# Kernel tuning notes

Measured on AMD Instinct MI355X. Metric: run time of the kernel, lower is better.

The kernel has to match this reference:

```python
import jax, jax.numpy as jnp
import numpy as np

B, T, C, H = 128, 256, 384, 6
HS = C // H  # 64
EPS = 1e-5


def _ln(x, g, b):
    mu = jnp.mean(x, axis=-1, keepdims=True)
    var = jnp.mean(jnp.square(x - mu), axis=-1, keepdims=True)
    return (x - mu) * jax.lax.rsqrt(var + EPS) * g + b


def setup_inputs() -> dict:
    key = jax.random.key(0)
    ks = jax.random.split(key, 12)
    s = 0.02
    return {
        "x": jax.random.normal(ks[0], (B, T, C), jnp.float32),
        "wq": jax.random.normal(ks[1], (H, C, HS), jnp.float32) * s,
        "wk": jax.random.normal(ks[2], (H, C, HS), jnp.float32) * s,
        "wv": jax.random.normal(ks[3], (H, C, HS), jnp.float32) * s,
        "w_proj": jax.random.normal(ks[4], (C, C), jnp.float32) * s,
        "b_proj": jax.random.normal(ks[5], (C,), jnp.float32) * s,
        "w1": jax.random.normal(ks[6], (C, 4 * C), jnp.float32) * s,
        "b1": jax.random.normal(ks[7], (4 * C,), jnp.float32) * s,
        "w2": jax.random.normal(ks[8], (4 * C, C), jnp.float32) * s,
        "b2": jax.random.normal(ks[9], (C,), jnp.float32) * s,
        "ln1_g": 1.0 + jax.random.normal(ks[10], (C,), jnp.float32) * s,
        "ln1_b": jnp.zeros((C,), jnp.float32),
        "ln2_g": 1.0 + jax.random.normal(ks[11], (C,), jnp.float32) * s,
        "ln2_b": jnp.zeros((C,), jnp.float32),
    }


def reference(x, wq, wk, wv, w_proj, b_proj, w1, b1, w2, b2, ln1_g, ln1_b, ln2_g, ln2_b):
    # --- attention sublayer (dropout = identity, eval mode) ---
    h = _ln(x, ln1_g, ln1_b)                              # (B,T,C)
    q = jnp.einsum("btc,hcd->bhtd", h, wq)               # (B,H,T,HS)
    k = jnp.einsum("btc,hcd->bhtd", h, wk)
    v = jnp.einsum("btc,hcd->bhtd", h, wv)
    # NOTE: original scales by n_embed**-0.5 (C), not head_size**-0.5
    wei = jnp.einsum("bhtd,bhsd->bhts", q, k) * (C ** -0.5)  # (B,H,T,T)
    tril = jnp.tril(jnp.ones((T, T), bool))
    wei = jnp.where(tril, wei, -jnp.inf)
    # NOTE: original applies softmax over torch dim=1 of (B,T,T) = query axis
    wei = jax.nn.softmax(wei, axis=2)
    attn = jnp.einsum("bhts,bhsd->bhtd", wei, v)          # (B,H,T,HS)
    attn = attn.transpose(0, 2, 1, 3).reshape(B, T, C)    # head-concat order
    x = x + attn @ w_proj + b_proj
    # --- MLP sublayer ---
    h2 = _ln(x, ln2_g, ln2_b)
    x = x + jax.nn.relu(h2 @ w1 + b1) @ w2 + b2
    return x
```

## Files before the change

### kernel.cpp

```cpp
#include <hip/hip_runtime.h>

#define BB 128
#define TT 256
#define CCH 384
#define NHH 6
#define HSZ 64
#define BTT (BB*TT)
#define QKVLD 1152

typedef unsigned short u16;
typedef unsigned int   u32;
typedef __attribute__((ext_vector_type(8))) short  short8;
typedef __attribute__((ext_vector_type(4))) float  floatx4;

__device__ __forceinline__ u16 f2bf(float f) {
  union { float f; u32 i; } v; v.f = f; u32 x = v.i;
  return (u16)((x + 0x7fffu + ((x >> 16) & 1u)) >> 16);
}
__device__ __forceinline__ float bf2f(u16 w) {
  union { u32 i; float f; } v; v.i = ((u32)w) << 16; return v.f;
}

__device__ __forceinline__ void gll16(const u16* g, u16* l) {
  __builtin_amdgcn_global_load_lds((const __attribute__((address_space(1))) void*)g,
                                   (__attribute__((address_space(3))) void*)l, 16, 0, 0);
}

template <int INBF>
__global__ __launch_bounds__(256) void ln_kernel(const void* __restrict__ xv,
                                                 const float* __restrict__ g,
                                                 const float* __restrict__ b,
                                                 u16* __restrict__ out) {
  int row = blockIdx.x * 4 + (threadIdx.x >> 6);
  int lane = threadIdx.x & 63;
  float vals[6];
  float sum = 0.f;
  if (INBF) {
    const u16* xr = (const u16*)xv + (size_t)row * CCH;
#pragma unroll
    for (int i = 0; i < 6; ++i) { vals[i] = bf2f(xr[lane + (i << 6)]); sum += vals[i]; }
  } else {
    const float* xr = (const float*)xv + (size_t)row * CCH;
#pragma unroll
    for (int i = 0; i < 6; ++i) { vals[i] = xr[lane + (i << 6)]; sum += vals[i]; }
  }
#pragma unroll
  for (int off = 32; off; off >>= 1) sum += __shfl_xor(sum, off);
  float mean = sum * (1.f / 384.f);
  float vs = 0.f;
#pragma unroll
  for (int i = 0; i < 6; ++i) { float d = vals[i] - mean; vs += d * d; }
#pragma unroll
  for (int off = 32; off; off >>= 1) vs += __shfl_xor(vs, off);
  float rinv = rsqrtf(vs * (1.f / 384.f) + 1e-5f);
  u16* orow = out + (size_t)row * CCH;
#pragma unroll
  for (int i = 0; i < 6; ++i) {
    int c = lane + (i << 6);
    orow[c] = f2bf((vals[i] - mean) * rinv * g[c] + b[c]);
  }
}

__global__ __launch_bounds__(256) void prep_all(const float* __restrict__ wq,
                                                const float* __restrict__ wk,
                                                const float* __restrict__ wv,
                                                const float* __restrict__ wproj,
                                                const float* __restrict__ w1,
                                                const float* __restrict__ w2,
                                                u16* __restrict__ wqkv_t, u16* __restrict__ wp_t,
                                                u16* __restrict__ w1_t, u16* __restrict__ w2_t,
                                                const float* __restrict__ x,
                                                const float* __restrict__ ln1g,
                                                const float* __restrict__ ln1b,
                                                u16* __restrict__ h_out) {
  const int bidx = blockIdx.x;
  if (bidx < 6912) {
    int idx = bidx * 256 + threadIdx.x;
    const int S1 = 442368;
    const int S2 = S1 + 147456;
    const int S3 = S2 + 589824;
    const int S4 = S3 + 589824;
    if (idx < S1) {
      int i = idx, e = i & 7, l = (i >> 3) & 63, r = i >> 9;
      int kt = r % 12, nb = r / 12;
      int n = nb * 16 + (l & 15), k = kt * 32 + (l >> 4) * 8 + e;
      int sel = n / 384, nn = n % 384;
      size_t src = ((size_t)(nn >> 6) * 384 + k) * 64 + (nn & 63);
      float v = (sel == 0) ? wq[src] : (sel == 1) ? wk[src] : wv[src];
      wqkv_t[i] = f2bf(v);
    } else if (idx < S2) {
      int i = idx - S1, e = i & 7, l = (i >> 3) & 63, r = i >> 9;
      int kt = r % 12, nb = r / 12;
      int n = nb * 16 + (l & 15), k = kt * 32 + (l >> 4) * 8 + e;
      wp_t[i] = f2bf(wproj[(size_t)k * 384 + n]);
    } else if (idx < S3) {
      int i = idx - S2, e = i & 7, l = (i >> 3) & 63, r = i >> 9;
      int kt = r % 12, nb = r / 12;
      int n = nb * 16 + (l & 15), k = kt * 32 + (l >> 4) * 8 + e;
      w1_t[i] = f2bf(w1[(size_t)k * 1536 + n]);
    } else if (idx < S4) {
      int i = idx - S3, e = i & 7, l = (i >> 3) & 63, r = i >> 9;
      int kt = r % 48, nb = r / 48;
      int n = nb * 16 + (l & 15), k = kt * 32 + (l >> 4) * 8 + e;
      w2_t[i] = f2bf(w2[(size_t)k * 384 + n]);
    }
  } else {
    int row = (bidx - 6912) * 4 + (threadIdx.x >> 6);
    int lane = threadIdx.x & 63;
    const float* xr = x + (size_t)row * CCH;
    float vals[6];
    float sum = 0.f;
#pragma unroll
    for (int i = 0; i < 6; ++i) { vals[i] = xr[lane + (i << 6)]; sum += vals[i]; }
#pragma unroll
    for (int off = 32; off; off >>= 1) sum += __shfl_xor(sum, off);
    float mean = sum * (1.f / 384.f);
    float vs = 0.f;
#pragma unroll
    for (int i = 0; i < 6; ++i) { float d = vals[i] - mean; vs += d * d; }
#pragma unroll
    for (int off = 32; off; off >>= 1) vs += __shfl_xor(vs, off);
    float rinv = rsqrtf(vs * (1.f / 384.f) + 1e-5f);
    u16* orow = h_out + (size_t)row * CCH;
#pragma unroll
    for (int i = 0; i < 6; ++i) {
      int c = lane + (i << 6);
      orow[c] = f2bf((vals[i] - mean) * rinv * ln1g[c] + ln1b[c]);
    }
  }
}

template <int BIAS, int RES, int RELU, int OUTBF, int RESBF>
__global__ __launch_bounds__(192, 2) void gemm_kres3(const u16* __restrict__ A,
                                                     const u16* __restrict__ Bp,
                                                     const float* __restrict__ bias,
                                                     const void* __restrict__ resv,
                                                     void* __restrict__ outv,
                                                     int M, int N) {
  __shared__ __align__(16) u16 Ah[12 * 2048];
  const int tid = threadIdx.x;
  const int lane = tid & 63;
  const int w = tid >> 6;

  const int gx = gridDim.x;
  const int nwg = gx * gridDim.y;
  const int bid = blockIdx.y * gx + blockIdx.x;
  const int lin = (bid & 7) * (nwg >> 3) + (bid >> 3);
  const int m0 = (lin / gx) * 64, n0 = (lin % gx) * 192;

  const int lm = lane & 15, qd = lane >> 4;

#pragma unroll
  for (int g = 0; g < 16; ++g) {
    int call = w * 16 + g;
    int kt = call >> 2, c = call & 3;
    int row = 16 * c + (lane >> 2);
    int ch = (lane & 3) ^ ((row >> 1) & 3);
    const u16* src = A + (size_t)(m0 + row) * 384 + kt * 32 + ch * 8;
    gll16(src, &Ah[kt * 2048 + c * 512]);
  }

  const u16* bsrc[4];
#pragma unroll
  for (int j = 0; j < 4; ++j)
    bsrc[j] = Bp + ((size_t)((n0 >> 4) + 4 * w + j) * 12) * 512 + lane * 8;

  floatx4 acc[4][4];
  floatx4 zero4 = {0.f, 0.f, 0.f, 0.f};
#pragma unroll
  for (int i = 0; i < 4; ++i)
#pragma unroll
    for (int j = 0; j < 4; ++j) acc[i][j] = zero4;

  short8 bf[4][4];
#pragma unroll
  for (int j = 0; j < 4; ++j) bf[0][j] = *(const short8*)(bsrc[j]);
#pragma unroll
  for (int j = 0; j < 4; ++j) bf[1][j] = *(const short8*)(bsrc[j] + 512);
#pragma unroll
  for (int j = 0; j < 4; ++j) bf[2][j] = *(const short8*)(bsrc[j] + 1024);

  asm volatile("s_waitcnt vmcnt(0)" ::: "memory");
  __syncthreads();

#pragma unroll
  for (int kt = 0; kt < 12; ++kt) {
    if (kt + 3 < 12) {
      const int pb = (kt + 3) & 3;
#pragma unroll
      for (int j = 0; j < 4; ++j)
        bf[pb][j] = *(const short8*)(bsrc[j] + (kt + 3) * 512);
    }
    const int cb = kt & 3;
    short8 af[4];
#pragma unroll
    for (int i = 0; i < 4; ++i) {
      int rm = 16 * i + lm;
      af[i] = *(const short8*)&Ah[kt * 2048 + rm * 32 + (qd ^ ((rm >> 1) & 3)) * 8];
    }
#pragma unroll
    for (int i = 0; i < 4; ++i)
#pragma unroll
      for (int j = 0; j < 4; ++j)
        acc[i][j] = __builtin_amdgcn_mfma_f32_16x16x32_bf16(af[i], bf[cb][j], acc[i][j], 0, 0, 0);
  }

#pragma unroll
  for (int i = 0; i < 4; ++i) {
    int row0 = m0 + 16 * i + qd * 4;
#pragma unroll
    for (int j = 0; j < 4; ++j) {
      int col = n0 + 64 * w + 16 * j + lm;
      float bb = 0.f;
      if (BIAS) bb = bias[col];
#pragma unroll
      for (int r = 0; r < 4; ++r) {
        size_t idx = (size_t)(row0 + r) * N + col;
        float val = acc[i][j][r] + bb;
        if (RES) val += RESBF ? bf2f(((const u16*)resv)[idx]) : ((const float*)resv)[idx];
        if (RELU) val = fmaxf(val, 0.f);
        if (OUTBF) ((u16*)outv)[idx] = f2bf(val);
        else       ((float*)outv)[idx] = val;
      }
    }
  }
}

template <int BIAS, int RES, int RELU, int OUTBF, int RESBF>
__global__ __launch_bounds__(256, 3) void gemm_mfma(const u16* __restrict__ A,
                                                    const u16* __restrict__ Bp,
                                                    const float* __restrict__ bias,
                                                    const void* __restrict__ resv,
                                                    void* __restrict__ outv,
                                                    int M, int N, int K) {
  __shared__ __align__(16) u16 As[2][128 * 32];
  const int tid = threadIdx.x;
  const int lane = tid & 63;
  const int w = tid >> 6;
  const int wr = w >> 1, wc = w & 1;

  const int gx = gridDim.x;
  const int nwg = gx * gridDim.y;
  const int bid = blockIdx.y * gx + blockIdx.x;
  const int lin = (bid & 7) * (nwg >> 3) + (bid >> 3);
  const int m0 = (lin / gx) * 128, n0 = (lin % gx) * 128;

  const int lm = lane & 15, qd = lane >> 4;
  const int KT = K >> 5;

  floatx4 acc[4][4];
  floatx4 zero4 = {0.f, 0.f, 0.f, 0.f};
#pragma unroll
  for (int i = 0; i < 4; ++i)
#pragma unroll
    for (int j = 0; j < 4; ++j) acc[i][j] = zero4;

  const u16* srcA[2];
#pragma unroll
  for (int c = 0; c < 2; ++c) {
    int row = 32 * w + 16 * c + (lane >> 2);
    int ch = (lane & 3) ^ ((row >> 1) & 3);
    srcA[c] = A + (size_t)(m0 + row) * K + ch * 8;
  }
  const int dA = (32 * w) * 32;

  const u16* bsrc[4];
#pragma unroll
  for (int j = 0; j < 4; ++j)
    bsrc[j] = Bp + ((size_t)((n0 >> 4) + 4 * wc + j) * KT) * 512 + lane * 8;

#pragma unroll
  for (int c = 0; c < 2; ++c) gll16(srcA[c], &As[0][dA + 512 * c]);
  short8 bcur[4], bnxt[4];
#pragma unroll
  for (int j = 0; j < 4; ++j) bcur[j] = *(const short8*)(bsrc[j]);

  for (int k0 = 0; k0 < K; k0 += 64) {
    __syncthreads();
    {
      int kn = k0 + 32;
      int kto = (kn >> 5) << 9;
#pragma unroll
      for (int j = 0; j < 4; ++j) bnxt[j] = *(const short8*)(bsrc[j] + kto);
#pragma unroll
      for (int c = 0; c < 2; ++c) gll16(srcA[c] + kn, &As[1][dA + 512 * c]);
      short8 af[4];
#pragma unroll
      for (int i = 0; i < 4; ++i) {
        int rm = 64 * wr + 16 * i + lm;
        af[i] = *(const short8*)&As[0][rm * 32 + (qd ^ ((rm >> 1) & 3)) * 8];
      }
#pragma unroll
      for (int i = 0; i < 4; ++i)
#pragma unroll
        for (int j = 0; j < 4; ++j)
          acc[i][j] = __builtin_amdgcn_mfma_f32_16x16x32_bf16(af[i], bcur[j], acc[i][j], 0, 0, 0);
    }
    __syncthreads();
    {
      int kn = k0 + 64;
      if (kn < K) {
        int kto = (kn >> 5) << 9;
#pragma unroll
        for (int j = 0; j < 4; ++j) bcur[j] = *(const short8*)(bsrc[j] + kto);
#pragma unroll
        for (int c = 0; c < 2; ++c) gll16(srcA[c] + kn, &As[0][dA + 512 * c]);
      }
      short8 af[4];
#pragma unroll
      for (int i = 0; i < 4; ++i) {
        int rm = 64 * wr + 16 * i + lm;
        af[i] = *(const short8*)&As[1][rm * 32 + (qd ^ ((rm >> 1) & 3)) * 8];
      }
#pragma unroll
      for (int i = 0; i < 4; ++i)
#pragma unroll
        for (int j = 0; j < 4; ++j)
          acc[i][j] = __builtin_amdgcn_mfma_f32_16x16x32_bf16(af[i], bnxt[j], acc[i][j], 0, 0, 0);
    }
  }

#pragma unroll
  for (int i = 0; i < 4; ++i) {
    int row0 = m0 + 64 * wr + 16 * i + qd * 4;
#pragma unroll
    for (int j = 0; j < 4; ++j) {
      int col = n0 + 64 * wc + 16 * j + lm;
      float bb = 0.f;
      if (BIAS) bb = bias[col];
#pragma unroll
      for (int r = 0; r < 4; ++r) {
        size_t idx = (size_t)(row0 + r) * N + col;
        float val = acc[i][j][r] + bb;
        if (RES) val += RESBF ? bf2f(((const u16*)resv)[idx]) : ((const float*)resv)[idx];
        if (RELU) val = fmaxf(val, 0.f);
        if (OUTBF) ((u16*)outv)[idx] = f2bf(val);
        else       ((float*)outv)[idx] = val;
      }
    }
  }
}

#define ASCALE 0.051031036307982884f

__global__ __launch_bounds__(1024) void attn_mfma(const u16* __restrict__ qkv,
                                                  u16* __restrict__ out) {
  __shared__ __align__(16) char lds_raw[36864 + 20480 + 2048];
  u16*   Ks       = (u16*)lds_raw;
  u16*   VT       = (u16*)lds_raw;
  float* partials = (float*)(lds_raw + 36864);
  u16*   stage    = (u16*)(lds_raw + 36864);
  float* gmax     = (float*)(lds_raw + 57344);
  float* linv     = (float*)(lds_raw + 58368);

  const int tid = threadIdx.x;
  const int lane = tid & 63;
  const int w = tid >> 6;
  const int lm = lane & 15, qd = lane >> 4;
  const int b = blockIdx.x / NHH, h = blockIdx.x % NHH;
  const size_t rowbase = (size_t)b * TT;
  const u16* qp = qkv + rowbase * QKVLD + h * HSZ;
  const u16* kp = qp + 384;
  const u16* vp = qp + 768;

  {
    int s = tid >> 2, c4 = tid & 3;
    const u16* src = kp + (size_t)s * QKVLD;
    *(uint4*)&Ks[s * 72 + c4 * 8]       = *(const uint4*)(src + c4 * 8);
    *(uint4*)&Ks[s * 72 + (c4 + 4) * 8] = *(const uint4*)(src + (c4 + 4) * 8);
  }
  short8 qf0, qf1;
  {
    const u16* qrow = qp + (size_t)(16 * w + lm) * QKVLD + qd * 8;
    qf0 = *(const short8*)(qrow);
    qf1 = *(const short8*)(qrow + 32);
  }
  __syncthreads();

  floatx4 acc[16];
  floatx4 zero4 = {0.f, 0.f, 0.f, 0.f};
#pragma unroll
  for (int tc = 0; tc < 16; ++tc) acc[tc] = zero4;

#pragma unroll
  for (int tc = 0; tc < 16; ++tc) {
    if (tc <= w) {
      int sr = 16 * tc + lm;
      short8 kf0 = *(const short8*)&Ks[sr * 72 + qd * 8];
      short8 kf1 = *(const short8*)&Ks[sr * 72 + 32 + qd * 8];
      acc[tc] = __builtin_amdgcn_mfma_f32_16x16x32_bf16(qf0, kf0, acc[tc], 0, 0, 0);
      acc[tc] = __builtin_amdgcn_mfma_f32_16x16x32_bf16(qf1, kf1, acc[tc], 0, 0, 0);
    }
  }

  const int rb = 16 * w + qd * 4;
  float pmax[16];
#pragma unroll
  for (int tc = 0; tc < 16; ++tc) {
    float m = -1e30f;
    if (tc <= w) {
      int sc = 16 * tc + lm;
#pragma unroll
      for (int r = 0; r < 4; ++r) {
        float vv = acc[tc][r] * ASCALE;
        vv = (rb + r >= sc) ? vv : -1e30f;
        acc[tc][r] = vv;
        m = fmaxf(m, vv);
      }
    }
    m = fmaxf(m, __shfl_xor(m, 16));
    m = fmaxf(m, __shfl_xor(m, 32));
    pmax[tc] = m;
  }
  if (lane < 16) {
#pragma unroll
    for (int tc = 0; tc < 16; ++tc) partials[w * 256 + tc * 16 + lane] = pmax[tc];
  }
  __syncthreads();
  if (tid < 256) {
    float m = partials[tid];
#pragma unroll
    for (int i = 1; i < 16; ++i) m = fmaxf(m, partials[i * 256 + tid]);
    gmax[tid] = m;
  }
  __syncthreads();

  float psum[16];
#pragma unroll
  for (int tc = 0; tc < 16; ++tc) {
    float s = 0.f;
    if (tc <= w) {
      float gm = gmax[tc * 16 + lm];
#pragma unroll
      for (int r = 0; r < 4; ++r) {
        float e = (acc[tc][r] > -1e29f) ? __expf(acc[tc][r] - gm) : 0.f;
        acc[tc][r] = e;
        s += e;
      }
    }
    s += __shfl_xor(s, 16);
    s += __shfl_xor(s, 32);
    psum[tc] = s;
  }
  if (lane < 16) {
#pragma unroll
    for (int tc = 0; tc < 16; ++tc) partials[w * 256 + tc * 16 + lane] = psum[tc];
  }
  __syncthreads();
  if (tid < 256) {
    float s = partials[tid];
#pragma unroll
    for (int i = 1; i < 16; ++i) s += partials[i * 256 + tid];
    linv[tid] = 1.f / s;
  }
  __syncthreads();

  {
    int s = tid >> 2, dg = (tid & 3) * 16;
    const u16* vrow = vp + (size_t)s * QKVLD + dg;
    u16 tmp[16];
    *(uint4*)&tmp[0] = *(const uint4*)(vrow);
    *(uint4*)&tmp[8] = *(const uint4*)(vrow + 8);
#pragma unroll
    for (int j = 0; j < 16; ++j) VT[(dg + j) * 264 + s] = tmp[j];
  }
  __syncthreads();

  u16* mst = stage + w * 640;
  floatx4 oacc[4];
#pragma unroll
  for (int nt = 0; nt < 4; ++nt) oacc[nt] = zero4;

#pragma unroll
  for (int c = 0; c < 8; ++c) {
    if (2 * c <= w) {
#pragma unroll
      for (int tt = 0; tt < 2; ++tt) {
        int tc = 2 * c + tt;
        float li = (tc <= w) ? linv[tc * 16 + lm] : 0.f;
#pragma unroll
        for (int r = 0; r < 4; ++r) {
          float pv = (tc <= w) ? acc[tc][r] * li : 0.f;
          mst[(qd * 4 + r) * 40 + tt * 16 + lm] = f2bf(pv);
        }
      }
      asm volatile("s_waitcnt lgkmcnt(0)" ::: "memory");
      short8 pf = *(const short8*)&mst[lm * 40 + qd * 8];
#pragma unroll
      for (int nt = 0; nt < 4; ++nt) {
        short8 vf = *(const short8*)&VT[(nt * 16 + lm) * 264 + c * 32 + qd * 8];
        oacc[nt] = __builtin_amdgcn_mfma_f32_16x16x32_bf16(pf, vf, oacc[nt], 0, 0, 0);
      }
      asm volatile("" ::: "memory");
    }
  }

  u16* ob = out + rowbase * CCH + h * HSZ;
#pragma unroll
  for (int nt = 0; nt < 4; ++nt) {
#pragma unroll
    for (int r = 0; r < 4; ++r) {
      int t = 16 * w + qd * 4 + r;
      ob[(size_t)t * CCH + nt * 16 + lm] = f2bf(oacc[nt][r]);
    }
  }
}

extern "C" void kernel_launch(void* const* d_in, const int* in_sizes, int n_in,
                              void* d_out, int out_size, void* d_ws, size_t ws_size,
                              hipStream_t stream) {
  const float* x     = (const float*)d_in[0];
  const float* wq    = (const float*)d_in[1];
  const float* wk    = (const float*)d_in[2];
  const float* wv    = (const float*)d_in[3];
  const float* wproj = (const float*)d_in[4];
  const float* bproj = (const float*)d_in[5];
  const float* w1    = (const float*)d_in[6];
  const float* b1    = (const float*)d_in[7];
  const float* w2    = (const float*)d_in[8];
  const float* b2    = (const float*)d_in[9];
  const float* ln1g  = (const float*)d_in[10];
  const float* ln1b  = (const float*)d_in[11];
  const float* ln2g  = (const float*)d_in[12];
  const float* ln2b  = (const float*)d_in[13];
  float* out = (float*)d_out;
  (void)in_sizes; (void)n_in; (void)out_size; (void)ws_size;

  char* ws = (char*)d_ws;
  size_t off = 0;
  auto alloc = [&](size_t bytes) -> void* {
    void* p = ws + off;
    off += (bytes + 255) & ~(size_t)255;
    return p;
  };

  u16* wqkv_t = (u16*)alloc((size_t)QKVLD * CCH * 2);
  u16* wp_t   = (u16*)alloc((size_t)CCH * CCH * 2);
  u16* w1_t   = (u16*)alloc((size_t)4 * CCH * CCH * 2);
  u16* w2_t   = (u16*)alloc((size_t)CCH * 4 * CCH * 2);
  u16*   h_b  = (u16*)alloc((size_t)BTT * CCH * 2);
  u16*   x2   = (u16*)alloc((size_t)BTT * CCH * 2);
  u16*   qkv_b = (u16*)alloc((size_t)BTT * 4 * CCH * 2);
  u16*   u_b   = qkv_b;

  prep_all<<<15104, 256, 0, stream>>>(wq, wk, wv, wproj, w1, w2,
                                      wqkv_t, wp_t, w1_t, w2_t,
                                      x, ln1g, ln1b, h_b);

  gemm_kres3<0, 0, 0, 1, 0><<<dim3(6, 512), 192, 0, stream>>>(h_b, wqkv_t, nullptr, nullptr,
                                                              qkv_b, BTT, QKVLD);
  attn_mfma<<<BB * NHH, 1024, 0, stream>>>(qkv_b, h_b);

  gemm_kres3<1, 1, 0, 1, 0><<<dim3(2, 512), 192, 0, stream>>>(h_b, wp_t, bproj, x, x2,
                                                              BTT, CCH);
  ln_kernel<1><<<BTT / 4, 256, 0, stream>>>(x2, ln2g, ln2b, h_b);

  gemm_kres3<1, 0, 1, 1, 0><<<dim3(8, 512), 192, 0, stream>>>(h_b, w1_t, b1, nullptr, u_b,
                                                              BTT, 4 * CCH);
  gemm_mfma<1, 1, 0, 0, 1><<<dim3(3, 256), 256, 0, stream>>>(u_b, w2_t, b2, x2, out,
                                                             BTT, CCH, 4 * CCH);
}
```

Baseline: 335.0 us.

## Fold LayerNorm into GEMM epilogues via precomputed column sums and row stats

```diff
diff --git a/kernel.cpp b/kernel.cpp
--- a/kernel.cpp
+++ b/kernel.cpp
@@ -20,45 +20,11 @@
 __device__ __forceinline__ float bf2f(u16 w) {
   union { u32 i; float f; } v; v.i = ((u32)w) << 16; return v.f;
 }
+__device__ __forceinline__ float rndbf(float f) { return bf2f(f2bf(f)); }
 
 __device__ __forceinline__ void gll16(const u16* g, u16* l) {
   __builtin_amdgcn_global_load_lds((const __attribute__((address_space(1))) void*)g,
                                    (__attribute__((address_space(3))) void*)l, 16, 0, 0);
-}
-
-template <int INBF>
-__global__ __launch_bounds__(256) void ln_kernel(const void* __restrict__ xv,
-                                                 const float* __restrict__ g,
-                                                 const float* __restrict__ b,
-                                                 u16* __restrict__ out) {
-  int row = blockIdx.x * 4 + (threadIdx.x >> 6);
-  int lane = threadIdx.x & 63;
-  float vals[6];
-  float sum = 0.f;
-  if (INBF) {
-    const u16* xr = (const u16*)xv + (size_t)row * CCH;
-#pragma unroll
-    for (int i = 0; i < 6; ++i) { vals[i] = bf2f(xr[lane + (i << 6)]); sum += vals[i]; }
-  } else {
-    const float* xr = (const float*)xv + (size_t)row * CCH;
-#pragma unroll
-    for (int i = 0; i < 6; ++i) { vals[i] = xr[lane + (i << 6)]; sum += vals[i]; }
-  }
-#pragma unroll
-  for (int off = 32; off; off >>= 1) sum += __shfl_xor(sum, off);
-  float mean = sum * (1.f / 384.f);
-  float vs = 0.f;
-#pragma unroll
-  for (int i = 0; i < 6; ++i) { float d = vals[i] - mean; vs += d * d; }
-#pragma unroll
-  for (int off = 32; off; off >>= 1) vs += __shfl_xor(vs, off);
-  float rinv = rsqrtf(vs * (1.f / 384.f) + 1e-5f);
-  u16* orow = out + (size_t)row * CCH;
-#pragma unroll
-  for (int i = 0; i < 6; ++i) {
-    int c = lane + (i << 6);
-    orow[c] = f2bf((vals[i] - mean) * rinv * g[c] + b[c]);
-  }
 }
 
 __global__ __launch_bounds__(256) void prep_all(const float* __restrict__ wq,
@@ -72,7 +38,12 @@
                                                 const float* __restrict__ x,
                                                 const float* __restrict__ ln1g,
                                                 const float* __restrict__ ln1b,
-                                                u16* __restrict__ h_out) {
+                                                const float* __restrict__ ln2g,
+                                                const float* __restrict__ ln2b,
+                                                u16* __restrict__ xb,
+                                                float* __restrict__ st1,
+                                                float* __restrict__ c1q, float* __restrict__ c2q,
+                                                float* __restrict__ c1m, float* __restrict__ c2m) {
   const int bidx = blockIdx.x;
   if (bidx < 6912) {
     int idx = bidx * 256 + threadIdx.x;
@@ -87,7 +58,7 @@
       int sel = n / 384, nn = n % 384;
       size_t src = ((size_t)(nn >> 6) * 384 + k) * 64 + (nn & 63);
       float v = (sel == 0) ? wq[src] : (sel == 1) ? wk[src] : wv[src];
-      wqkv_t[i] = f2bf(v);
+      wqkv_t[i] = f2bf(ln1g[k] * v);
     } else if (idx < S2) {
       int i = idx - S1, e = i & 7, l = (i >> 3) & 63, r = i >> 9;
       int kt = r % 12, nb = r / 12;
@@ -97,14 +68,14 @@
       int i = idx - S2, e = i & 7, l = (i >> 3) & 63, r = i >> 9;
       int kt = r % 12, nb = r / 12;
       int n = nb * 16 + (l & 15), k = kt * 32 + (l >> 4) * 8 + e;
-      w1_t[i] = f2bf(w1[(size_t)k * 1536 + n]);
+      w1_t[i] = f2bf(ln2g[k] * w1[(size_t)k * 1536 + n]);
     } else if (idx < S4) {
       int i = idx - S3, e = i & 7, l = (i >> 3) & 63, r = i >> 9;
       int kt = r % 48, nb = r / 48;
       int n = nb * 16 + (l & 15), k = kt * 32 + (l >> 4) * 8 + e;
       w2_t[i] = f2bf(w2[(size_t)k * 384 + n]);
     }
-  } else {
+  } else if (bidx < 15104) {
     int row = (bidx - 6912) * 4 + (threadIdx.x >> 6);
     int lane = threadIdx.x & 63;
     const float* xr = x + (size_t)row * CCH;
@@ -121,23 +92,56 @@
 #pragma unroll
     for (int off = 32; off; off >>= 1) vs += __shfl_xor(vs, off);
     float rinv = rsqrtf(vs * (1.f / 384.f) + 1e-5f);
-    u16* orow = h_out + (size_t)row * CCH;
-#pragma unroll
-    for (int i = 0; i < 6; ++i) {
-      int c = lane + (i << 6);
-      orow[c] = f2bf((vals[i] - mean) * rinv * ln1g[c] + ln1b[c]);
-    }
-  }
-}
-
-template <int BIAS, int RES, int RELU, int OUTBF, int RESBF>
+    u16* orow = xb + (size_t)row * CCH;
+#pragma unroll
+    for (int i = 0; i < 6; ++i) orow[lane + (i << 6)] = f2bf(vals[i]);
+    if (lane == 0) { st1[2 * row] = mean; st1[2 * row + 1] = rinv; }
+  } else {
+    int col = (bidx - 15104) * 4 + (threadIdx.x >> 6);
+    int lane = threadIdx.x & 63;
+    float s1 = 0.f, s2 = 0.f;
+    if (col < 1152) {
+      int sel = col / 384, nn = col % 384;
+      const float* wsel = (sel == 0) ? wq : (sel == 1) ? wk : wv;
+#pragma unroll
+      for (int i = 0; i < 6; ++i) {
+        int k = lane + (i << 6);
+        float v = wsel[((size_t)(nn >> 6) * 384 + k) * 64 + (nn & 63)];
+        s1 += rndbf(ln1g[k] * v);
+        s2 += ln1b[k] * v;
+      }
+#pragma unroll
+      for (int off = 32; off; off >>= 1) { s1 += __shfl_xor(s1, off); s2 += __shfl_xor(s2, off); }
+      if (lane == 0) { c1q[col] = s1; c2q[col] = s2; }
+    } else {
+      int n = col - 1152;
+#pragma unroll
+      for (int i = 0; i < 6; ++i) {
+        int k = lane + (i << 6);
+        float v = w1[(size_t)k * 1536 + n];
+        s1 += rndbf(ln2g[k] * v);
+        s2 += ln2b[k] * v;
+      }
+#pragma unroll
+      for (int off = 32; off; off >>= 1) { s1 += __shfl_xor(s1, off); s2 += __shfl_xor(s2, off); }
+      if (lane == 0) { c1m[n] = s1; c2m[n] = s2; }
+    }
+  }
+}
+
+template <int BIAS, int RES, int RELU, int OUTBF, int RESBF, int LNFOLD, int STATSOUT>
 __global__ __launch_bounds__(192, 2) void gemm_kres3(const u16* __restrict__ A,
                                                      const u16* __restrict__ Bp,
                                                      const float* __restrict__ bias,
                                                      const void* __restrict__ resv,
                                                      void* __restrict__ outv,
-                                                     int M, int N) {
+                                                     int M, int N,
+                                                     const float* __restrict__ stin,
+                                                     float* __restrict__ stout,
+                                                     const float* __restrict__ c1,
+                                                     const float* __restrict__ c2) {
   __shared__ __align__(16) u16 Ah[12 * 2048];
+  __shared__ float wpart[64][4][2];
   const int tid = threadIdx.x;
   const int lane = tid & 63;
   const int w = tid >> 6;
@@ -172,26 +176,24 @@
 #pragma unroll
     for (int j = 0; j < 4; ++j) acc[i][j] = zero4;
 
-  short8 bf[4][4];
+  short8 bf[3][4];
 #pragma unroll
   for (int j = 0; j < 4; ++j) bf[0][j] = *(const short8*)(bsrc[j]);
 #pragma unroll
   for (int j = 0; j < 4; ++j) bf[1][j] = *(const short8*)(bsrc[j] + 512);
-#pragma unroll
-  for (int j = 0; j < 4; ++j) bf[2][j] = *(const short8*)(bsrc[j] + 1024);
 
   asm volatile("s_waitcnt vmcnt(0)" ::: "memory");
   __syncthreads();
 
 #pragma unroll
   for (int kt = 0; kt < 12; ++kt) {
-    if (kt + 3 < 12) {
-      const int pb = (kt + 3) & 3;
+    if (kt + 2 < 12) {
+      const int pb = (kt + 2) % 3;
 #pragma unroll
       for (int j = 0; j < 4; ++j)
-        bf[pb][j] = *(const short8*)(bsrc[j] + (kt + 3) * 512);
-    }
-    const int cb = kt & 3;
+        bf[pb][j] = *(const short8*)(bsrc[j] + (kt + 2) * 512);
+    }
+    const int cb = kt % 3;
     short8 af[4];
 #pragma unroll
     for (int i = 0; i < 4; ++i) {
@@ -205,23 +207,79 @@
         acc[i][j] = __builtin_amdgcn_mfma_f32_16x16x32_bf16(af[i], bf[cb][j], acc[i][j], 0, 0, 0);
   }
 
+  float rs[4][4], rq[4][4];
 #pragma unroll
   for (int i = 0; i < 4; ++i) {
     int row0 = m0 + 16 * i + qd * 4;
+    float mu_[4], ri_[4];
+    if (LNFOLD == 1) {
+#pragma unroll
+      for (int r = 0; r < 4; ++r) {
+        mu_[r] = stin[2 * (row0 + r)];
+        ri_[r] = stin[2 * (row0 + r) + 1];
+      }
+    } else if (LNFOLD == 2) {
+#pragma unroll
+      for (int r = 0; r < 4; ++r) {
+        float p0 = stin[(row0 + r) * 4 + 0], q0 = stin[(row0 + r) * 4 + 1];
+        float p1 = stin[(row0 + r) * 4 + 2], q1 = stin[(row0 + r) * 4 + 3];
+        float mu = (p0 + p1) * (1.f / 384.f);
+        float var = (q0 + q1) * (1.f / 384.f) - mu * mu;
+        mu_[r] = mu;
+        ri_[r] = rsqrtf(var + 1e-5f);
+      }
+    }
+    if (STATSOUT) {
+#pragma unroll
+      for (int r = 0; r < 4; ++r) { rs[i][r] = 0.f; rq[i][r] = 0.f; }
+    }
 #pragma unroll
     for (int j = 0; j < 4; ++j) {
       int col = n0 + 64 * w + 16 * j + lm;
       float bb = 0.f;
       if (BIAS) bb = bias[col];
+      float c1v = 0.f, c2v = 0.f;
+      if (LNFOLD) { c1v = c1[col]; c2v = c2[col]; }
 #pragma unroll
       for (int r = 0; r < 4; ++r) {
         size_t idx = (size_t)(row0 + r) * N + col;
-        float val = acc[i][j][r] + bb;
+        float val;
+        if (LNFOLD) val = ri_[r] * (acc[i][j][r] - mu_[r] * c1v) + c2v + bb;
+        else        val = acc[i][j][r] + bb;
         if (RES) val += RESBF ? bf2f(((const u16*)resv)[idx]) : ((const float*)resv)[idx];
         if (RELU) val = fmaxf(val, 0.f);
+        if (STATSOUT) { rs[i][r] += val; rq[i][r] += val * val; }
         if (OUTBF) ((u16*)outv)[idx] = f2bf(val);
         else       ((float*)outv)[idx] = val;
       }
+    }
+  }
+
+  if (STATSOUT) {
+    const int cbk = n0 / 192 & 1;
+#pragma unroll
+    for (int i = 0; i < 4; ++i) {
+#pragma unroll
+      for (int r = 0; r < 4; ++r) {
+        float s = rs[i][r], q = rq[i][r];
+#pragma unroll
+        for (int off = 1; off < 16; off <<= 1) {
+          s += __shfl_xor(s, off);
+          q += __shfl_xor(q, off);
+        }
+        if (lm == 0) {
+          int rl = 16 * i + qd * 4 + r;
+          wpart[rl][w][0] = s;
+          wpart[rl][w][1] = q;
+        }
+      }
+    }
+    __syncthreads();
+    if (tid < 64) {
+      float S = wpart[tid][0][0] + wpart[tid][1][0] + wpart[tid][2][0];
+      float Q = wpart[tid][0][1] + wpart[tid][1][1] + wpart[tid][2][1];
+      stout[(size_t)(m0 + tid) * 4 + cbk * 2 + 0] = S;
+      stout[(size_t)(m0 + tid) * 4 + cbk * 2 + 1] = Q;
     }
   }
 }
@@ -538,25 +596,34 @@
   u16* wp_t   = (u16*)alloc((size_t)CCH * CCH * 2);
   u16* w1_t   = (u16*)alloc((size_t)4 * CCH * CCH * 2);
   u16* w2_t   = (u16*)alloc((size_t)CCH * 4 * CCH * 2);
+  u16*   xb   = (u16*)alloc((size_t)BTT * CCH * 2);
   u16*   h_b  = (u16*)alloc((size_t)BTT * CCH * 2);
   u16*   x2   = (u16*)alloc((size_t)BTT * CCH * 2);
   u16*   qkv_b = (u16*)alloc((size_t)BTT * 4 * CCH * 2);
   u16*   u_b   = qkv_b;
-
-  prep_all<<<15104, 256, 0, stream>>>(wq, wk, wv, wproj, w1, w2,
+  float* st1  = (float*)alloc((size_t)BTT * 2 * 4);
+  float* st2p = (float*)alloc((size_t)BTT * 4 * 4);
+  float* c1q  = (float*)alloc(1152 * 4);
+  float* c2q  = (float*)alloc(1152 * 4);
+  float* c1m  = (float*)alloc(1536 * 4);
+  float* c2m  = (float*)alloc(1536 * 4);
+
+  prep_all<<<15776, 256, 0, stream>>>(wq, wk, wv, wproj, w1, w2,
                                       wqkv_t, wp_t, w1_t, w2_t,
-                                      x, ln1g, ln1b, h_b);
-
-  gemm_kres3<0, 0, 0, 1, 0><<<dim3(6, 512), 192, 0, stream>>>(h_b, wqkv_t, nullptr, nullptr,
-                                                              qkv_b, BTT, QKVLD);
+                                      x, ln1g, ln1b, ln2g, ln2b,
+                                      xb, st1, c1q, c2q, c1m, c2m);
+
+  gemm_kres3<0, 0, 0, 1, 0, 1, 0><<<dim3(6, 512), 192, 0, stream>>>(
+      xb, wqkv_t, nullptr, nullptr, qkv_b, BTT, QKVLD, st1, nullptr, c1q, c2q);
+
   attn_mfma<<<BB * NHH, 1024, 0, stream>>>(qkv_b, h_b);
 
-  gemm_kres3<1, 1, 0, 1, 0><<<dim3(2, 512), 192, 0, stream>>>(h_b, wp_t, bproj, x, x2,
-                                                              BTT, CCH);
-  ln_kernel<1><<<BTT / 4, 256, 0, stream>>>(x2, ln2g, ln2b, h_b);
-
-  gemm_kres3<1, 0, 1, 1, 0><<<dim3(8, 512), 192, 0, stream>>>(h_b, w1_t, b1, nullptr, u_b,
-                                                              BTT, 4 * CCH);
+  gemm_kres3<1, 1, 0, 1, 0, 0, 1><<<dim3(2, 512), 192, 0, stream>>>(
+      h_b, wp_t, bproj, x, x2, BTT, CCH, nullptr, st2p, nullptr, nullptr);
+
+  gemm_kres3<1, 0, 1, 1, 0, 2, 0><<<dim3(8, 512), 192, 0, stream>>>(
+      x2, w1_t, b1, nullptr, u_b, BTT, 4 * CCH, st2p, nullptr, c1m, c2m);
+
   gemm_mfma<1, 1, 0, 0, 1><<<dim3(3, 256), 256, 0, stream>>>(u_b, w2_t, b2, x2, out,
                                                              BTT, CCH, 4 * CCH);
 }
```

Result: slower. 366.3 us (+9.4%).
